# Optimization experiments

Hardware: AMD Instinct MI355X
Metric: run time of the kernel (lower is better)

The kernel has to match this reference:

```python
import jax, jax.numpy as jnp
import numpy as np

B, N, E, H = 4, 2048, 256, 8
D = E // H
EPS = 1e-5


def _layernorm(x, g, b):
    mu = jnp.mean(x, axis=-1, keepdims=True)
    var = jnp.mean(jnp.square(x - mu), axis=-1, keepdims=True)
    return (x - mu) * jax.lax.rsqrt(var + EPS) * g + b


def setup_inputs() -> dict:
    key = jax.random.key(0)
    ks = jax.random.split(key, 8)
    s = 1.0 / np.sqrt(E)
    lin = lambda k: (jax.random.normal(k, (E, E), jnp.float32) * s)
    return {
        "x_l": jax.random.normal(ks[0], (B, N, E), jnp.float32),
        "x_r": jax.random.normal(ks[1], (B, N, E), jnp.float32),
        "Wq": lin(ks[2]), "bq": jnp.zeros((E,), jnp.float32),
        "Wk": lin(ks[3]), "bk": jnp.zeros((E,), jnp.float32),
        "Wv": lin(ks[4]), "bv": jnp.zeros((E,), jnp.float32),
        "Wp": lin(ks[5]), "bp": jnp.zeros((E,), jnp.float32),
        "ln_g": jnp.ones((E,), jnp.float32), "ln_b": jnp.zeros((E,), jnp.float32),
        "rn_g": jnp.ones((E,), jnp.float32), "rn_b": jnp.zeros((E,), jnp.float32),
    }


def reference(x_l, x_r, Wq, bq, Wk, bk, Wv, bv, Wp, bp, ln_g, ln_b, rn_g, rn_b):
    # projections -> [b, h, n, d]
    q = (x_l @ Wq + bq).reshape(B, N, H, D).transpose(0, 2, 1, 3)
    k = (x_r @ Wk + bk).reshape(B, N, H, D).transpose(0, 2, 1, 3)
    # shared value from the difference of the two streams
    v = ((x_l - x_r) @ Wv + bv).reshape(B, N, H, D).transpose(0, 2, 1, 3)

    energy = jnp.einsum('bhqd,bhkd->bhqk', q, k)  # [b,h,n,n]
    attn = jax.nn.softmax(energy / np.sqrt(D), axis=-1)  # dropout p=0 (eval)

    # attn used as-is and transposed against the SAME value tensor
    out_l = jnp.einsum('bhqk,bhkd->bhqd', attn, v)
    out_r = jnp.einsum('bhqk,bhqd->bhkd', attn, v)  # == attn^T @ v

    out_l = out_l.transpose(0, 2, 1, 3).reshape(B, N, E)
    out_r = out_r.transpose(0, 2, 1, 3).reshape(B, N, E)

    out_l = _layernorm(out_l @ Wp + bp, ln_g, ln_b) + x_l
    out_r = _layernorm(out_r @ Wp + bp, rn_g, rn_b) + x_r
    return (out_l, out_r)
```

## Files before the change

### kernel.cpp

```cpp
#include <hip/hip_runtime.h>
#include <math.h>


typedef __attribute__((ext_vector_type(8))) short short8;
typedef __attribute__((ext_vector_type(4))) float f32x4;
typedef __attribute__((ext_vector_type(16))) float f32x16;
typedef __attribute__((ext_vector_type(4))) unsigned short u16x4;

union FragU { unsigned int u[4]; short8 s8; };

__device__ __forceinline__ unsigned short bf16_rn(float f) {
    union { float f; unsigned int u; } c; c.f = f;
    return (unsigned short)((c.u + 0x7FFFu + ((c.u >> 16) & 1u)) >> 16);
}
__device__ __forceinline__ float b2f(unsigned short u) {
    union { unsigned int i; float f; } c; c.i = ((unsigned int)u) << 16;
    return c.f;
}

#if __has_builtin(__builtin_amdgcn_exp2f)
__device__ __forceinline__ float fexp2(float x) { return __builtin_amdgcn_exp2f(x); }
#else
__device__ __forceinline__ float fexp2(float x) { return exp2f(x); }
#endif

__device__ __forceinline__ f32x4 mfma16(short8 a, short8 b, f32x4 c) {
    return __builtin_amdgcn_mfma_f32_16x16x32_bf16(a, b, c, 0, 0, 0);
}
__device__ __forceinline__ f32x16 mfma32(short8 a, short8 b, f32x16 c) {
    return __builtin_amdgcn_mfma_f32_32x32x16_bf16(a, b, c, 0, 0, 0);
}

__device__ __forceinline__ void plswap(unsigned int& x, unsigned int& y) {
    asm("v_permlane32_swap_b32 %0, %1" : "+v"(x), "+v"(y));
}

__device__ __forceinline__ short8 pfrag(unsigned int w0, unsigned int w1,
                                        unsigned int w2, unsigned int w3) {
    plswap(w0, w2);
    plswap(w1, w3);
    FragU fu;
    fu.u[0] = w0; fu.u[1] = w1; fu.u[2] = w2; fu.u[3] = w3;
    return fu.s8;
}

__global__ void prep_all(const float* __restrict__ xl, const float* __restrict__ xr,
                         const float* __restrict__ Wq, const float* __restrict__ Wk,
                         const float* __restrict__ Wv, const float* __restrict__ Wp,
                         unsigned short* __restrict__ xlb, unsigned short* __restrict__ xrb,
                         unsigned short* __restrict__ xdb,
                         unsigned short* __restrict__ Wqt, unsigned short* __restrict__ Wkt,
                         unsigned short* __restrict__ Wvt, unsigned short* __restrict__ Wpt) {
    const int bid = blockIdx.x;
    if (bid < 2048) {
        const size_t i = ((size_t)bid * 256 + threadIdx.x) * 4;
        const float4 A = *(const float4*)(xl + i);
        const float4 Bv = *(const float4*)(xr + i);
        u16x4 pa = { bf16_rn(A.x), bf16_rn(A.y), bf16_rn(A.z), bf16_rn(A.w) };
        u16x4 pb = { bf16_rn(Bv.x), bf16_rn(Bv.y), bf16_rn(Bv.z), bf16_rn(Bv.w) };
        u16x4 pd = { bf16_rn(A.x - Bv.x), bf16_rn(A.y - Bv.y),
                     bf16_rn(A.z - Bv.z), bf16_rn(A.w - Bv.w) };
        *(u16x4*)(xlb + i) = pa;
        *(u16x4*)(xrb + i) = pb;
        *(u16x4*)(xdb + i) = pd;
    } else {
        const int gid = (bid - 2048) * 256 + threadIdx.x;
        const int m = gid >> 16;
        const int idx = gid & 65535;
        const int k = idx >> 8, n = idx & 255;
        const float* W = (m == 0) ? Wq : (m == 1) ? Wk : (m == 2) ? Wv : Wp;
        unsigned short* Wt = (m == 0) ? Wqt : (m == 1) ? Wkt : (m == 2) ? Wvt : Wpt;
        Wt[n * 256 + k] = bf16_rn(W[(size_t)k * 256 + n]);
    }
}

__launch_bounds__(256)
__global__ void qkv_gemm(const unsigned short* __restrict__ xlb,
                         const unsigned short* __restrict__ xrb,
                         const unsigned short* __restrict__ xdb,
                         const unsigned short* __restrict__ Wqt,
                         const unsigned short* __restrict__ Wkt,
                         const unsigned short* __restrict__ Wvt,
                         const float* __restrict__ bq, const float* __restrict__ bk,
                         const float* __restrict__ bv,
                         unsigned short* __restrict__ Qg, unsigned short* __restrict__ Kg,
                         unsigned short* __restrict__ Vtg) {
    const int z = blockIdx.z;
    const unsigned short* A  = (z == 0) ? xlb : (z == 1) ? xrb : xdb;
    const unsigned short* Wt = (z == 0) ? Wqt : (z == 1) ? Wkt : Wvt;
    const float* bias        = (z == 0) ? bq  : (z == 1) ? bk  : bv;

    __shared__ unsigned short At[2][128][40];
    __shared__ unsigned short Bt[2][64][40];

    const int tid = threadIdx.x;
    const int lane = tid & 63, wv = tid >> 6;
    const int a = lane & 15, g = lane >> 4;
    const int wr = wv >> 1, wc = wv & 1;
    const int r0 = blockIdx.x * 128;
    const int c0 = blockIdx.y * 64;

    const f32x4 fz = {0.f, 0.f, 0.f, 0.f};
    f32x4 acc[4][2];
#pragma unroll
    for (int f = 0; f < 4; ++f)
#pragma unroll
        for (int t = 0; t < 2; ++t) acc[f][t] = fz;

    const int arow = tid >> 1, aoff = (tid & 1) * 16;
    const int brow = tid >> 2, boff = (tid & 3) * 8;
    const unsigned short* asrc = A + (size_t)(r0 + arow) * 256 + aoff;
    const unsigned short* bsrc = Wt + (size_t)(c0 + brow) * 256 + boff;

#define QKV_STAGE(KS, BUF)                                                      \
    {                                                                           \
        *(short8*)&At[BUF][arow][aoff]     = *(const short8*)(asrc + (KS) * 32); \
        *(short8*)&At[BUF][arow][aoff + 8] = *(const short8*)(asrc + (KS) * 32 + 8); \
        *(short8*)&Bt[BUF][brow][boff]     = *(const short8*)(bsrc + (KS) * 32); \
    }

    QKV_STAGE(0, 0)
    __syncthreads();

#pragma unroll
    for (int ks = 0; ks < 8; ++ks) {
        const int b = ks & 1;
        if (ks < 7) QKV_STAGE(ks + 1, b ^ 1)
        short8 af[4], bfr[2];
#pragma unroll
        for (int f = 0; f < 4; ++f) af[f] = *(const short8*)&At[b][wr * 64 + f * 16 + a][g * 8];
#pragma unroll
        for (int t = 0; t < 2; ++t) bfr[t] = *(const short8*)&Bt[b][wc * 32 + t * 16 + a][g * 8];
#pragma unroll
        for (int f = 0; f < 4; ++f)
#pragma unroll
            for (int t = 0; t < 2; ++t) acc[f][t] = mfma16(af[f], bfr[t], acc[f][t]);
        __syncthreads();
    }
#undef QKV_STAGE

    const float scq = 0.17677669529663687f * 1.4426950408889634f;
#pragma unroll
    for (int t = 0; t < 2; ++t) {
        const int C = c0 + wc * 32 + t * 16 + a;
        const float bb = bias[C];
        const int h = C >> 5, d = C & 31;
#pragma unroll
        for (int f = 0; f < 4; ++f) {
            const int Rb = r0 + wr * 64 + f * 16 + g * 4;
            const int b_ = Rb >> 11, n = Rb & 2047;
            const int bhh = b_ * 8 + h;
            float v[4];
#pragma unroll
            for (int r = 0; r < 4; ++r) {
                v[r] = acc[f][t][r] + bb;
                if (z == 0) v[r] *= scq;
            }
            if (z < 2) {
                unsigned short* dst = ((z == 0) ? Qg : Kg) + (size_t)(bhh * 2048 + n) * 32 + d;
#pragma unroll
                for (int r = 0; r < 4; ++r) dst[(size_t)r * 32] = bf16_rn(v[r]);
            } else {
                u16x4 pk = { bf16_rn(v[0]), bf16_rn(v[1]), bf16_rn(v[2]), bf16_rn(v[3]) };
                *(u16x4*)(Vtg + (size_t)(bhh * 32 + d) * 2048 + n) = pk;
            }
        }
    }
}

#define P1_TILE(SB)                                                             \
    {                                                                           \
        const short8 ck0 = *(const short8*)((SB) + ro);                         \
        const short8 ck1 = *(const short8*)((SB) + 512 + ro);                   \
        const short8 cv0 = *(const short8*)((SB) + 1024 + ro);                  \
        const short8 cv1 = *(const short8*)((SB) + 1536 + ro);                  \
        f32x16 s = {};                                                          \
        s = mfma32(ck0, qf0, s);                                                \
        s = mfma32(ck1, qf1, s);                                                \
        float p[16];                                                            \
        _Pragma("unroll") for (int j = 0; j < 16; ++j) p[j] = fexp2(s[j]);      \
        l_run += (((p[0] + p[1]) + (p[2] + p[3])) + ((p[4] + p[5]) + (p[6] + p[7]))) \
               + (((p[8] + p[9]) + (p[10] + p[11])) + ((p[12] + p[13]) + (p[14] + p[15]))); \
        unsigned int w[8];                                                      \
        _Pragma("unroll") for (int mm = 0; mm < 8; ++mm)                        \
            asm("v_cvt_pk_bf16_f32 %0, %1, %2"                                  \
                : "=v"(w[mm]) : "v"(p[2 * mm]), "v"(p[2 * mm + 1]));            \
        acc = mfma32(cv0, pfrag(w[0], w[1], w[2], w[3]), acc);                  \
        acc = mfma32(cv1, pfrag(w[4], w[5], w[6], w[7]), acc);                  \
    }

__launch_bounds__(512, 4)
__global__ void attn_pass1(const unsigned short* __restrict__ Qg,
                           const unsigned short* __restrict__ Kg,
                           const unsigned short* __restrict__ Vtg,
                           unsigned short* __restrict__ AOl,
                           unsigned short* __restrict__ Vsg) {
    __shared__ unsigned short ST[2][2][2][2][2][64][8];
    __shared__ float accS[4][16][64];
    __shared__ float lsumS[4][64];

    const int f = blockIdx.x;
    const int bh = 4 * (f & 7) + (f >> 7);
    const int qblk = (f >> 3) & 15;
    const int tid = threadIdx.x;
    const int wv = tid >> 6;
    const int qi = wv & 3, z = wv >> 2;
    const int lane = tid & 63, l31 = lane & 31, hi = lane >> 5;
    const int q0 = qblk * 128 + qi * 32;

    const unsigned short* Qb = Qg + (size_t)bh * 2048 * 32;
    const unsigned short* Kb = Kg + (size_t)bh * 2048 * 32;
    const unsigned short* Vb = Vtg + (size_t)bh * 32 * 2048;

    const short8 qf0 = *(const short8*)(Qb + (size_t)(q0 + l31) * 32 + hi * 8);
    const short8 qf1 = *(const short8*)(Qb + (size_t)(q0 + l31) * 32 + 16 + hi * 8);

    const int kv = qi >> 1;
    const int srow = (qi & 1) * 16 + (lane >> 2);
    const int m = lane & 3;
    unsigned short* wp00 = &ST[z][0][0][kv][m >> 1][srow + 32 * (m & 1)][0];
    unsigned short* wp01 = &ST[z][0][1][kv][m >> 1][srow + 32 * (m & 1)][0];
    unsigned short* wp10 = &ST[z][1][0][kv][m >> 1][srow + 32 * (m & 1)][0];
    unsigned short* wp11 = &ST[z][1][1][kv][m >> 1][srow + 32 * (m & 1)][0];
    const size_t gstep = kv ? 32 : 1024;
    const unsigned short* sgb = kv
        ? Vb + (size_t)srow * 2048 + m * 8
        : Kb + (size_t)srow * 32 + m * 8;
    const int zt = z * 32;

    const unsigned short* rb00 = &ST[z][0][0][0][0][0][0];
    const unsigned short* rb01 = &ST[z][0][1][0][0][0][0];
    const unsigned short* rb10 = &ST[z][1][0][0][0][0][0];
    const unsigned short* rb11 = &ST[z][1][1][0][0][0][0];
    const int ro = (l31 + 32 * hi) * 8;

    f32x16 acc = {};
    float l_run = 0.f;

    short8 rr0 = *(const short8*)(sgb + (size_t)(zt + 0) * gstep);
    short8 rr1 = *(const short8*)(sgb + (size_t)(zt + 1) * gstep);
    *(short8*)wp00 = rr0;
    *(short8*)wp01 = rr1;
    rr0 = *(const short8*)(sgb + (size_t)(zt + 2) * gstep);
    rr1 = *(const short8*)(sgb + (size_t)(zt + 3) * gstep);
    __syncthreads();

#pragma unroll
    for (int ph = 0; ph < 16; ++ph) {
        const int pb = ph & 1;
        unsigned short* wA = pb ? wp00 : wp10;
        unsigned short* wB = pb ? wp01 : wp11;
        const unsigned short* rA = pb ? rb10 : rb00;
        const unsigned short* rB = pb ? rb11 : rb01;
        if (ph < 15) { *(short8*)wA = rr0; *(short8*)wB = rr1; }
        if (ph < 14) {
            rr0 = *(const short8*)(sgb + (size_t)(zt + 2 * ph + 4) * gstep);
            rr1 = *(const short8*)(sgb + (size_t)(zt + 2 * ph + 5) * gstep);
        }
        P1_TILE(rA)
        P1_TILE(rB)
        __syncthreads();
    }

    float lsum = l_run + __shfl_xor(l_run, 32);

    if (z == 1) {
#pragma unroll
        for (int j = 0; j < 16; ++j) accS[qi][j][lane] = acc[j];
        lsumS[qi][lane] = lsum;
    }
    __syncthreads();
    if (z == 0) {
        lsum += lsumS[qi][lane];
        const float rl = 1.0f / lsum;
#pragma unroll
        for (int j = 0; j < 16; ++j) acc[j] += accS[qi][j][lane];

        const int b_ = bh >> 3, h = bh & 7;
        const int q = q0 + l31;
        unsigned short* dst = AOl + (size_t)(b_ * 2048 + q) * 256 + h * 32;
#pragma unroll
        for (int g2 = 0; g2 < 4; ++g2) {
            u16x4 pk = { bf16_rn(acc[4 * g2 + 0] * rl), bf16_rn(acc[4 * g2 + 1] * rl),
                         bf16_rn(acc[4 * g2 + 2] * rl), bf16_rn(acc[4 * g2 + 3] * rl) };
            *(u16x4*)(dst + 8 * g2 + 4 * hi) = pk;
        }
        if (hi == 0) lsumS[qi][l31] = rl;
    }
    __syncthreads();
    if (z == 1) {
        const int cb = hi * 16;
        float il[16];
#pragma unroll
        for (int e = 0; e < 16; e += 4) {
            const float4 v4 = *(const float4*)&lsumS[qi][cb + e];
            il[e] = v4.x; il[e + 1] = v4.y; il[e + 2] = v4.z; il[e + 3] = v4.w;
        }
        const unsigned short* vsrc = Vb + (size_t)l31 * 2048 + q0 + cb;
        unsigned short* vdst = Vsg + (size_t)bh * 32 * 2048 + (size_t)l31 * 2048 + q0 + cb;
#pragma unroll
        for (int c4 = 0; c4 < 4; ++c4) {
            const u16x4 vv = *(const u16x4*)(vsrc + c4 * 4);
            u16x4 o = { bf16_rn(b2f(vv.x) * il[c4 * 4 + 0]),
                        bf16_rn(b2f(vv.y) * il[c4 * 4 + 1]),
                        bf16_rn(b2f(vv.z) * il[c4 * 4 + 2]),
                        bf16_rn(b2f(vv.w) * il[c4 * 4 + 3]) };
            *(u16x4*)(vdst + c4 * 4) = o;
        }
    }
}

#define P2_TILE(SB)                                                             \
    {                                                                           \
        const short8 cq0 = *(const short8*)((SB) + ro);                         \
        const short8 cq1 = *(const short8*)((SB) + 512 + ro);                   \
        const short8 cv0 = *(const short8*)((SB) + 1024 + ro);                  \
        const short8 cv1 = *(const short8*)((SB) + 1536 + ro);                  \
        f32x16 s = {};                                                          \
        s = mfma32(cq0, kf0, s);                                                \
        s = mfma32(cq1, kf1, s);                                                \
        float p[16];                                                            \
        _Pragma("unroll") for (int j = 0; j < 16; ++j) p[j] = fexp2(s[j]);      \
        unsigned int w[8];                                                      \
        _Pragma("unroll") for (int mm = 0; mm < 8; ++mm)                        \
            asm("v_cvt_pk_bf16_f32 %0, %1, %2"                                  \
                : "=v"(w[mm]) : "v"(p[2 * mm]), "v"(p[2 * mm + 1]));            \
        acc = mfma32(pfrag(w[0], w[1], w[2], w[3]), cv0, acc);                  \
        acc = mfma32(pfrag(w[4], w[5], w[6], w[7]), cv1, acc);                  \
    }

__launch_bounds__(512, 4)
__global__ void attn_pass2(const unsigned short* __restrict__ Qg,
                           const unsigned short* __restrict__ Kg,
                           const unsigned short* __restrict__ Vsg,
                           unsigned short* __restrict__ AOr) {
    __shared__ unsigned short ST[2][2][2][2][2][64][8];
    __shared__ float accS[4][16][64];

    const int f = blockIdx.x;
    const int bh = 4 * (f & 7) + (f >> 7);
    const int kblk = (f >> 3) & 15;
    const int tid = threadIdx.x;
    const int wv = tid >> 6;
    const int ki = wv & 3, z = wv >> 2;
    const int lane = tid & 63, l31 = lane & 31, hi = lane >> 5;
    const int k0 = kblk * 128 + ki * 32;

    const unsigned short* Qb = Qg + (size_t)bh * 2048 * 32;
    const unsigned short* Kb = Kg + (size_t)bh * 2048 * 32;
    const unsigned short* Vb = Vsg + (size_t)bh * 32 * 2048;

    const short8 kf0 = *(const short8*)(Kb + (size_t)(k0 + l31) * 32 + hi * 8);
    const short8 kf1 = *(const short8*)(Kb + (size_t)(k0 + l31) * 32 + 16 + hi * 8);

    const int kv = ki >> 1;
    const int srow = (ki & 1) * 16 + (lane >> 2);
    const int m = lane & 3;
    unsigned short* wp00 = &ST[z][0][0][kv][m >> 1][srow + 32 * (m & 1)][0];
    unsigned short* wp01 = &ST[z][0][1][kv][m >> 1][srow + 32 * (m & 1)][0];
    unsigned short* wp10 = &ST[z][1][0][kv][m >> 1][srow + 32 * (m & 1)][0];
    unsigned short* wp11 = &ST[z][1][1][kv][m >> 1][srow + 32 * (m & 1)][0];
    const size_t gstep = kv ? 32 : 1024;
    const unsigned short* sgb = kv
        ? Vb + (size_t)srow * 2048 + m * 8
        : Qb + (size_t)srow * 32 + m * 8;
    const int zt = z * 32;

    const unsigned short* rb00 = &ST[z][0][0][0][0][0][0];
    const unsigned short* rb01 = &ST[z][0][1][0][0][0][0];
    const unsigned short* rb10 = &ST[z][1][0][0][0][0][0];
    const unsigned short* rb11 = &ST[z][1][1][0][0][0][0];
    const int ro = (l31 + 32 * hi) * 8;

    f32x16 acc = {};

    short8 rr0 = *(const short8*)(sgb + (size_t)(zt + 0) * gstep);
    short8 rr1 = *(const short8*)(sgb + (size_t)(zt + 1) * gstep);
    *(short8*)wp00 = rr0;
    *(short8*)wp01 = rr1;
    rr0 = *(const short8*)(sgb + (size_t)(zt + 2) * gstep);
    rr1 = *(const short8*)(sgb + (size_t)(zt + 3) * gstep);
    __syncthreads();

#pragma unroll
    for (int ph = 0; ph < 16; ++ph) {
        const int pb = ph & 1;
        unsigned short* wA = pb ? wp00 : wp10;
        unsigned short* wB = pb ? wp01 : wp11;
        const unsigned short* rA = pb ? rb10 : rb00;
        const unsigned short* rB = pb ? rb11 : rb01;
        if (ph < 15) { *(short8*)wA = rr0; *(short8*)wB = rr1; }
        if (ph < 14) {
            rr0 = *(const short8*)(sgb + (size_t)(zt + 2 * ph + 4) * gstep);
            rr1 = *(const short8*)(sgb + (size_t)(zt + 2 * ph + 5) * gstep);
        }
        P2_TILE(rA)
        P2_TILE(rB)
        __syncthreads();
    }

    if (z == 1) {
#pragma unroll
        for (int j = 0; j < 16; ++j) accS[ki][j][lane] = acc[j];
    }
    __syncthreads();
    if (z == 0) {
#pragma unroll
        for (int j = 0; j < 16; ++j) acc[j] += accS[ki][j][lane];

        const int b_ = bh >> 3, h = bh & 7;
#pragma unroll
        for (int j = 0; j < 16; ++j) {
            const int krow = k0 + (j & 3) + 8 * (j >> 2) + 4 * hi;
            AOr[(size_t)(b_ * 2048 + krow) * 256 + h * 32 + l31] = bf16_rn(acc[j]);
        }
    }
}

__launch_bounds__(256)
__global__ void proj_ln(const unsigned short* __restrict__ AOl,
                        const unsigned short* __restrict__ AOr,
                        const unsigned short* __restrict__ Wpt,
                        const float* __restrict__ bp,
                        const float* __restrict__ ln_g, const float* __restrict__ ln_b,
                        const float* __restrict__ rn_g, const float* __restrict__ rn_b,
                        const float* __restrict__ xl, const float* __restrict__ xr,
                        float* __restrict__ out) {
    __shared__ unsigned short At[64][264];
    __shared__ unsigned short Bt[2][256][40];

    const int sel = blockIdx.y;
    const unsigned short* AO = sel ? AOr : AOl;
    const float* gamma = sel ? rn_g : ln_g;
    const float* beta  = sel ? rn_b : ln_b;
    const float* xres  = sel ? xr : xl;
    float* o = out + (size_t)sel * 8192 * 256;

    const int tid = threadIdx.x;
    const int lane = tid & 63, wv = tid >> 6;
    const int a = lane & 15, g = lane >> 4;
    const int r0 = blockIdx.x * 64;

    {
        const int row = tid >> 2, seg = (tid & 3) * 64;
        const unsigned short* src = AO + (size_t)(r0 + row) * 256 + seg;
#pragma unroll
        for (int i = 0; i < 8; ++i)
            *(short8*)&At[row][seg + i * 8] = *(const short8*)(src + i * 8);
    }
    const unsigned short* wsrc = Wpt + (size_t)tid * 256;
    {
#pragma unroll
        for (int i = 0; i < 4; ++i)
            *(short8*)&Bt[0][tid][i * 8] = *(const short8*)(wsrc + i * 8);
    }

    const f32x4 fz = {0.f, 0.f, 0.f, 0.f};
    f32x4 acc[16];
#pragma unroll
    for (int cf = 0; cf < 16; ++cf) acc[cf] = fz;

    __syncthreads();

#pragma unroll
    for (int ks = 0; ks < 8; ++ks) {
        const int b = ks & 1;
        if (ks < 7) {
#pragma unroll
            for (int i = 0; i < 4; ++i)
                *(short8*)&Bt[b ^ 1][tid][i * 8] =
                    *(const short8*)(wsrc + (ks + 1) * 32 + i * 8);
        }
        const short8 af = *(const short8*)&At[wv * 16 + a][ks * 32 + g * 8];
#pragma unroll
        for (int cf = 0; cf < 16; ++cf) {
            const short8 bfr = *(const short8*)&Bt[b][cf * 16 + a][g * 8];
            acc[cf] = mfma16(af, bfr, acc[cf]);
        }
        __syncthreads();
    }

    float bb[16], gg[16], be[16];
#pragma unroll
    for (int cf = 0; cf < 16; ++cf) {
        const int c = cf * 16 + a;
        bb[cf] = bp[c]; gg[cf] = gamma[c]; be[cf] = beta[c];
    }
#pragma unroll
    for (int r = 0; r < 4; ++r) {
        float y[16];
        float s1 = 0.f, s2 = 0.f;
#pragma unroll
        for (int cf = 0; cf < 16; ++cf) {
            y[cf] = acc[cf][r] + bb[cf];
            s1 += y[cf];
            s2 += y[cf] * y[cf];
        }
#pragma unroll
        for (int mask = 1; mask <= 8; mask <<= 1) {
            s1 += __shfl_xor(s1, mask);
            s2 += __shfl_xor(s2, mask);
        }
        const float mu = s1 * (1.0f / 256.0f);
        const float var = s2 * (1.0f / 256.0f) - mu * mu;
        const float rstd = rsqrtf(var + 1e-5f);
        const int R = r0 + wv * 16 + g * 4 + r;
#pragma unroll
        for (int cf = 0; cf < 16; ++cf) {
            const int c = cf * 16 + a;
            o[(size_t)R * 256 + c] =
                (y[cf] - mu) * rstd * gg[cf] + be[cf] + xres[(size_t)R * 256 + c];
        }
    }
}

extern "C" void kernel_launch(void* const* d_in, const int* in_sizes, int n_in,
                              void* d_out, int out_size, void* d_ws, size_t ws_size,
                              hipStream_t stream) {
    const float* x_l  = (const float*)d_in[0];
    const float* x_r  = (const float*)d_in[1];
    const float* Wq   = (const float*)d_in[2];
    const float* bq   = (const float*)d_in[3];
    const float* Wk   = (const float*)d_in[4];
    const float* bk   = (const float*)d_in[5];
    const float* Wv   = (const float*)d_in[6];
    const float* bv   = (const float*)d_in[7];
    const float* Wp   = (const float*)d_in[8];
    const float* bp   = (const float*)d_in[9];
    const float* ln_g = (const float*)d_in[10];
    const float* ln_b = (const float*)d_in[11];
    const float* rn_g = (const float*)d_in[12];
    const float* rn_b = (const float*)d_in[13];

    const size_t SZ_TOK = (size_t)8192 * 256;

    unsigned short* xl_bf = (unsigned short*)d_ws;
    unsigned short* xr_bf = xl_bf + SZ_TOK;
    unsigned short* xd_bf = xr_bf + SZ_TOK;
    unsigned short* Qg    = xd_bf + SZ_TOK;
    unsigned short* Kg    = Qg + SZ_TOK;
    unsigned short* Vtg   = Kg + SZ_TOK;
    unsigned short* Wqt   = Vtg + SZ_TOK;
    unsigned short* Wkt   = Wqt + 65536;
    unsigned short* Wvt   = Wkt + 65536;
    unsigned short* Wpt   = Wvt + 65536;
    unsigned short* AOl   = xl_bf;
    unsigned short* AOr   = xr_bf;
    unsigned short* Vs    = xd_bf;
    float* out = (float*)d_out;

    prep_all<<<3072, 256, 0, stream>>>(x_l, x_r, Wq, Wk, Wv, Wp,
                                       xl_bf, xr_bf, xd_bf, Wqt, Wkt, Wvt, Wpt);
    qkv_gemm<<<dim3(64, 4, 3), 256, 0, stream>>>(xl_bf, xr_bf, xd_bf,
                                                 Wqt, Wkt, Wvt, bq, bk, bv, Qg, Kg, Vtg);
    attn_pass1<<<512, 512, 0, stream>>>(Qg, Kg, Vtg, AOl, Vs);
    attn_pass2<<<512, 512, 0, stream>>>(Qg, Kg, Vs, AOr);
    proj_ln<<<dim3(128, 2), 256, 0, stream>>>(AOl, AOr, Wpt, bp,
                                              ln_g, ln_b, rn_g, rn_b, x_l, x_r, out);
}
```

Before: 90.37 us.

## Load GEMM A-fragments directly to registers, split attention accumulators, add setprio

```diff
diff --git a/kernel.cpp b/kernel.cpp
--- a/kernel.cpp
+++ b/kernel.cpp
@@ -90,7 +90,6 @@
     const unsigned short* Wt = (z == 0) ? Wqt : (z == 1) ? Wkt : Wvt;
     const float* bias        = (z == 0) ? bq  : (z == 1) ? bk  : bv;
 
-    __shared__ unsigned short At[2][128][40];
     __shared__ unsigned short Bt[2][64][40];
 
     const int tid = threadIdx.x;
@@ -107,37 +106,36 @@
 #pragma unroll
         for (int t = 0; t < 2; ++t) acc[f][t] = fz;
 
-    const int arow = tid >> 1, aoff = (tid & 1) * 16;
     const int brow = tid >> 2, boff = (tid & 3) * 8;
-    const unsigned short* asrc = A + (size_t)(r0 + arow) * 256 + aoff;
     const unsigned short* bsrc = Wt + (size_t)(c0 + brow) * 256 + boff;
-
-#define QKV_STAGE(KS, BUF)                                                      \
-    {                                                                           \
-        *(short8*)&At[BUF][arow][aoff]     = *(const short8*)(asrc + (KS) * 32); \
-        *(short8*)&At[BUF][arow][aoff + 8] = *(const short8*)(asrc + (KS) * 32 + 8); \
-        *(short8*)&Bt[BUF][brow][boff]     = *(const short8*)(bsrc + (KS) * 32); \
-    }
-
-    QKV_STAGE(0, 0)
+    const unsigned short* abase = A + (size_t)(r0 + wr * 64 + a) * 256 + g * 8;
+
+    short8 afA[4], afB[4];
+#pragma unroll
+    for (int f = 0; f < 4; ++f) afA[f] = *(const short8*)(abase + f * 16 * 256);
+    *(short8*)&Bt[0][brow][boff] = *(const short8*)bsrc;
     __syncthreads();
 
 #pragma unroll
     for (int ks = 0; ks < 8; ++ks) {
         const int b = ks & 1;
-        if (ks < 7) QKV_STAGE(ks + 1, b ^ 1)
-        short8 af[4], bfr[2];
-#pragma unroll
-        for (int f = 0; f < 4; ++f) af[f] = *(const short8*)&At[b][wr * 64 + f * 16 + a][g * 8];
+        const short8* afc = (ks & 1) ? afB : afA;
+        short8* afn = (ks & 1) ? afA : afB;
+        if (ks < 7) {
+            *(short8*)&Bt[b ^ 1][brow][boff] = *(const short8*)(bsrc + (ks + 1) * 32);
+#pragma unroll
+            for (int f = 0; f < 4; ++f)
+                afn[f] = *(const short8*)(abase + f * 16 * 256 + (ks + 1) * 32);
+        }
+        short8 bfr[2];
 #pragma unroll
         for (int t = 0; t < 2; ++t) bfr[t] = *(const short8*)&Bt[b][wc * 32 + t * 16 + a][g * 8];
 #pragma unroll
         for (int f = 0; f < 4; ++f)
 #pragma unroll
-            for (int t = 0; t < 2; ++t) acc[f][t] = mfma16(af[f], bfr[t], acc[f][t]);
+            for (int t = 0; t < 2; ++t) acc[f][t] = mfma16(afc[f], bfr[t], acc[f][t]);
         __syncthreads();
     }
-#undef QKV_STAGE
 
     const float scq = 0.17677669529663687f * 1.4426950408889634f;
 #pragma unroll
@@ -168,25 +166,29 @@
     }
 }
 
-#define P1_TILE(SB)                                                             \
+#define P1_TILE(SB, ACC, LRUN)                                                  \
     {                                                                           \
         const short8 ck0 = *(const short8*)((SB) + ro);                         \
         const short8 ck1 = *(const short8*)((SB) + 512 + ro);                   \
         const short8 cv0 = *(const short8*)((SB) + 1024 + ro);                  \
         const short8 cv1 = *(const short8*)((SB) + 1536 + ro);                  \
+        __builtin_amdgcn_s_setprio(1);                                          \
         f32x16 s = {};                                                          \
         s = mfma32(ck0, qf0, s);                                                \
         s = mfma32(ck1, qf1, s);                                                \
+        __builtin_amdgcn_s_setprio(0);                                          \
         float p[16];                                                            \
         _Pragma("unroll") for (int j = 0; j < 16; ++j) p[j] = fexp2(s[j]);      \
-        l_run += (((p[0] + p[1]) + (p[2] + p[3])) + ((p[4] + p[5]) + (p[6] + p[7]))) \
-               + (((p[8] + p[9]) + (p[10] + p[11])) + ((p[12] + p[13]) + (p[14] + p[15]))); \
+        LRUN += (((p[0] + p[1]) + (p[2] + p[3])) + ((p[4] + p[5]) + (p[6] + p[7]))) \
+              + (((p[8] + p[9]) + (p[10] + p[11])) + ((p[12] + p[13]) + (p[14] + p[15]))); \
         unsigned int w[8];                                                      \
         _Pragma("unroll") for (int mm = 0; mm < 8; ++mm)                        \
             asm("v_cvt_pk_bf16_f32 %0, %1, %2"                                  \
                 : "=v"(w[mm]) : "v"(p[2 * mm]), "v"(p[2 * mm + 1]));            \
-        acc = mfma32(cv0, pfrag(w[0], w[1], w[2], w[3]), acc);                  \
-        acc = mfma32(cv1, pfrag(w[4], w[5], w[6], w[7]), acc);                  \
+        __builtin_amdgcn_s_setprio(1);                                          \
+        ACC = mfma32(cv0, pfrag(w[0], w[1], w[2], w[3]), ACC);                  \
+        ACC = mfma32(cv1, pfrag(w[4], w[5], w[6], w[7]), ACC);                  \
+        __builtin_amdgcn_s_setprio(0);                                          \
     }
 
 __launch_bounds__(512, 4)
@@ -234,8 +236,8 @@
     const unsigned short* rb11 = &ST[z][1][1][0][0][0][0];
     const int ro = (l31 + 32 * hi) * 8;
 
-    f32x16 acc = {};
-    float l_run = 0.f;
+    f32x16 accA = {}, accB = {};
+    float l_runA = 0.f, l_runB = 0.f;
 
     short8 rr0 = *(const short8*)(sgb + (size_t)(zt + 0) * gstep);
     short8 rr1 = *(const short8*)(sgb + (size_t)(zt + 1) * gstep);
@@ -257,11 +259,20 @@
             rr0 = *(const short8*)(sgb + (size_t)(zt + 2 * ph + 4) * gstep);
             rr1 = *(const short8*)(sgb + (size_t)(zt + 2 * ph + 5) * gstep);
         }
-        P1_TILE(rA)
-        P1_TILE(rB)
+        if (qi & 1) {
+            P1_TILE(rB, accB, l_runB)
+            P1_TILE(rA, accA, l_runA)
+        } else {
+            P1_TILE(rA, accA, l_runA)
+            P1_TILE(rB, accB, l_runB)
+        }
         __syncthreads();
     }
 
+    f32x16 acc;
+#pragma unroll
+    for (int j = 0; j < 16; ++j) acc[j] = accA[j] + accB[j];
+    const float l_run = l_runA + l_runB;
     float lsum = l_run + __shfl_xor(l_run, 32);
 
     if (z == 1) {
@@ -310,23 +321,27 @@
     }
 }
 
-#define P2_TILE(SB)                                                             \
+#define P2_TILE(SB, ACC)                                                        \
     {                                                                           \
         const short8 cq0 = *(const short8*)((SB) + ro);                         \
         const short8 cq1 = *(const short8*)((SB) + 512 + ro);                   \
         const short8 cv0 = *(const short8*)((SB) + 1024 + ro);                  \
         const short8 cv1 = *(const short8*)((SB) + 1536 + ro);                  \
+        __builtin_amdgcn_s_setprio(1);                                          \
         f32x16 s = {};                                                          \
         s = mfma32(cq0, kf0, s);                                                \
         s = mfma32(cq1, kf1, s);                                                \
+        __builtin_amdgcn_s_setprio(0);                                          \
         float p[16];                                                            \
         _Pragma("unroll") for (int j = 0; j < 16; ++j) p[j] = fexp2(s[j]);      \
         unsigned int w[8];                                                      \
         _Pragma("unroll") for (int mm = 0; mm < 8; ++mm)                        \
             asm("v_cvt_pk_bf16_f32 %0, %1, %2"                                  \
                 : "=v"(w[mm]) : "v"(p[2 * mm]), "v"(p[2 * mm + 1]));            \
-        acc = mfma32(pfrag(w[0], w[1], w[2], w[3]), cv0, acc);                  \
-        acc = mfma32(pfrag(w[4], w[5], w[6], w[7]), cv1, acc);                  \
+        __builtin_amdgcn_s_setprio(1);                                          \
+        ACC = mfma32(pfrag(w[0], w[1], w[2], w[3]), cv0, ACC);                  \
+        ACC = mfma32(pfrag(w[4], w[5], w[6], w[7]), cv1, ACC);                  \
+        __builtin_amdgcn_s_setprio(0);                                          \
     }
 
 __launch_bounds__(512, 4)
@@ -372,7 +387,7 @@
     const unsigned short* rb11 = &ST[z][1][1][0][0][0][0];
     const int ro = (l31 + 32 * hi) * 8;
 
-    f32x16 acc = {};
+    f32x16 accA = {}, accB = {};
 
     short8 rr0 = *(const short8*)(sgb + (size_t)(zt + 0) * gstep);
     short8 rr1 = *(const short8*)(sgb + (size_t)(zt + 1) * gstep);
@@ -394,10 +409,19 @@
             rr0 = *(const short8*)(sgb + (size_t)(zt + 2 * ph + 4) * gstep);
             rr1 = *(const short8*)(sgb + (size_t)(zt + 2 * ph + 5) * gstep);
         }
-        P2_TILE(rA)
-        P2_TILE(rB)
+        if (ki & 1) {
+            P2_TILE(rB, accB)
+            P2_TILE(rA, accA)
+        } else {
+            P2_TILE(rA, accA)
+            P2_TILE(rB, accB)
+        }
         __syncthreads();
     }
+
+    f32x16 acc;
+#pragma unroll
+    for (int j = 0; j < 16; ++j) acc[j] = accA[j] + accB[j];
 
     if (z == 1) {
 #pragma unroll
@@ -426,7 +450,6 @@
                         const float* __restrict__ rn_g, const float* __restrict__ rn_b,
                         const float* __restrict__ xl, const float* __restrict__ xr,
                         float* __restrict__ out) {
-    __shared__ unsigned short At[64][264];
     __shared__ unsigned short Bt[2][256][40];
 
     const int sel = blockIdx.y;
@@ -441,19 +464,19 @@
     const int a = lane & 15, g = lane >> 4;
     const int r0 = blockIdx.x * 64;
 
-    {
-        const int row = tid >> 2, seg = (tid & 3) * 64;
-        const unsigned short* src = AO + (size_t)(r0 + row) * 256 + seg;
-#pragma unroll
-        for (int i = 0; i < 8; ++i)
-            *(short8*)&At[row][seg + i * 8] = *(const short8*)(src + i * 8);
-    }
+    const unsigned short* asrc = AO + (size_t)(r0 + wv * 16 + a) * 256 + g * 8;
+    short8 af[8];
+#pragma unroll
+    for (int ks = 0; ks < 8; ++ks) af[ks] = *(const short8*)(asrc + ks * 32);
+
     const unsigned short* wsrc = Wpt + (size_t)tid * 256;
-    {
-#pragma unroll
-        for (int i = 0; i < 4; ++i)
-            *(short8*)&Bt[0][tid][i * 8] = *(const short8*)(wsrc + i * 8);
-    }
+    short8 st[4];
+#pragma unroll
+    for (int i = 0; i < 4; ++i) st[i] = *(const short8*)(wsrc + i * 8);
+#pragma unroll
+    for (int i = 0; i < 4; ++i) *(short8*)&Bt[0][tid][i * 8] = st[i];
+#pragma unroll
+    for (int i = 0; i < 4; ++i) st[i] = *(const short8*)(wsrc + 32 + i * 8);
 
     const f32x4 fz = {0.f, 0.f, 0.f, 0.f};
     f32x4 acc[16];
@@ -467,15 +490,17 @@
         const int b = ks & 1;
         if (ks < 7) {
 #pragma unroll
-            for (int i = 0; i < 4; ++i)
-                *(short8*)&Bt[b ^ 1][tid][i * 8] =
-                    *(const short8*)(wsrc + (ks + 1) * 32 + i * 8);
-        }
-        const short8 af = *(const short8*)&At[wv * 16 + a][ks * 32 + g * 8];
+            for (int i = 0; i < 4; ++i) *(short8*)&Bt[b ^ 1][tid][i * 8] = st[i];
+            if (ks < 6) {
+#pragma unroll
+                for (int i = 0; i < 4; ++i)
+                    st[i] = *(const short8*)(wsrc + (ks + 2) * 32 + i * 8);
+            }
+        }
 #pragma unroll
         for (int cf = 0; cf < 16; ++cf) {
             const short8 bfr = *(const short8*)&Bt[b][cf * 16 + a][g * 8];
-            acc[cf] = mfma16(af, bfr, acc[cf]);
+            acc[cf] = mfma16(af[ks], bfr, acc[cf]);
         }
         __syncthreads();
     }
```

Result: slower. 114.0 us (+26.2%).
